# Optimization experiments

Measured on AMD Instinct MI355X. Metric: run time of the kernel, lower is better.

The kernel has to match this reference:

```python
import jax, jax.numpy as jnp
import numpy as np

BETA = 0.5
THR = 1.0
BN_EPS = 1e-5

@jax.custom_vjp
def spike(x):
    # heaviside fire: spk = 1[x > 0]
    return (x > 0).astype(x.dtype)

def _spike_fwd(x):
    return spike(x), x

def _spike_bwd(x, g):
    # snnTorch surrogate.atan(), alpha=2: grad = (alpha/2) / (1 + (pi/2*alpha*x)^2) = 1/(1+(pi*x)^2)
    return (g / (1.0 + (jnp.pi * x) ** 2),)

spike.defvjp(_spike_fwd, _spike_bwd)

def setup_inputs() -> dict:
    key = jax.random.key(0)
    ks = jax.random.split(key, 6)
    B, T, D, O = 512, 128, 512, 10
    data = jax.random.normal(ks[0], (B, T, D), dtype=jnp.float32)
    # deterministic Dropout(0.5) mask in {0, 2} (scaled by 1/keep_prob), time-major
    u = jax.random.uniform(ks[1], (T, B, D), dtype=jnp.float32)
    drop_mask = (u > 0.5).astype(jnp.float32) * 2.0
    W1 = jax.random.normal(ks[2], (D, D), dtype=jnp.float32) / np.sqrt(D)
    b1 = jax.random.normal(ks[3], (D,), dtype=jnp.float32) * 0.01
    gamma = jnp.ones((D,), dtype=jnp.float32)
    bn_beta = jnp.zeros((D,), dtype=jnp.float32)
    W2 = jax.random.normal(ks[4], (O, D), dtype=jnp.float32) / np.sqrt(D)
    b2 = jax.random.normal(ks[5], (O,), dtype=jnp.float32) * 0.01
    return {"data": data, "drop_mask": drop_mask, "W1": W1, "b1": b1,
            "gamma": gamma, "bn_beta": bn_beta, "W2": W2, "b2": b2}

def reference(data, drop_mask, W1, b1, gamma, bn_beta, W2, b2):
    B, T, D = data.shape
    O = W2.shape[0]
    xs = jnp.transpose(data, (1, 0, 2))  # [T, B, D] time-major

    def batchnorm(x):  # training-mode BatchNorm1d over batch dim
        mean = jnp.mean(x, axis=0)
        var = jnp.mean((x - mean) ** 2, axis=0)
        return gamma * (x - mean) * jax.lax.rsqrt(var + BN_EPS) + bn_beta

    def step(carry, inp):
        mem1, spk1, mem2, spk2 = carry
        xt, mt = inp
        cur1 = batchnorm((mt * xt) @ W1.T + b1)          # dropout -> linear -> BN
        mem1 = BETA * mem1 + cur1 - spk1 * THR           # Leaky, subtract reset
        spk1 = spike(mem1 - THR)
        cur2 = spk1 @ W2.T + b2
        mem2 = BETA * mem2 + cur2 - spk2 * THR
        spk2 = spike(mem2 - THR)
        return (mem1, spk1, mem2, spk2), spk2

    init = (jnp.zeros((B, D), data.dtype), jnp.zeros((B, D), data.dtype),
            jnp.zeros((B, O), data.dtype), jnp.zeros((B, O), data.dtype))
    _, spk_rec = jax.lax.scan(step, init, (xs, drop_mask))
    return spk_rec  # [T, B, out_size] == torch.stack(spk_rec)
```

## Files before the change

### kernel.cpp

```cpp
#include <hip/hip_runtime.h>
#include <math.h>

#define B_ 512
#define T_ 128
#define D_ 512
#define O_ 10

typedef unsigned int uint32;
typedef unsigned long long uint64;
typedef short bf16x8 __attribute__((ext_vector_type(8)));
typedef float f32x4 __attribute__((ext_vector_type(4)));

__device__ __forceinline__ uint32 bf16rne(float f) {
    uint32 u = __float_as_uint(f);
    return (u + 0x7FFFu + ((u >> 16) & 1u)) >> 16;
}
__device__ __forceinline__ float bf16f(uint32 h) { return __uint_as_float(h << 16); }

__device__ __forceinline__ uint32 pkbf16(float lo, float hi) {
    return bf16rne(lo) | (bf16rne(hi) << 16);
}

__device__ __forceinline__ void gload16_lds(const void* g, void* l) {
    __builtin_amdgcn_global_load_lds(
        (const __attribute__((address_space(1))) unsigned int*)g,
        (__attribute__((address_space(3))) unsigned int*)l, 16, 0, 0);
}

__global__ __launch_bounds__(256)
void presplitW_kernel(const float* __restrict__ W1, unsigned short* __restrict__ Wsp)
{
    const int idx = blockIdx.x * 256 + threadIdx.x;
    const float4 v = *(const float4*)(W1 + (size_t)idx * 4);
    float vv[4] = {v.x, v.y, v.z, v.w};
    uint32 c0[4], c1[4], c2[4];
#pragma unroll
    for (int i = 0; i < 4; ++i) {
        c0[i] = bf16rne(vv[i]);
        float r = vv[i] - bf16f(c0[i]);
        c1[i] = bf16rne(r);
        float r2 = r - bf16f(c1[i]);
        c2[i] = bf16rne(r2);
    }
    const size_t base = (size_t)idx * 4;
    uint2 w;
    w.x = c0[0] | (c0[1] << 16); w.y = c0[2] | (c0[3] << 16);
    *(uint2*)(Wsp + base) = w;
    w.x = c1[0] | (c1[1] << 16); w.y = c1[2] | (c1[3] << 16);
    *(uint2*)(Wsp + 262144 + base) = w;
    w.x = c2[0] | (c2[1] << 16); w.y = c2[2] | (c2[3] << 16);
    *(uint2*)(Wsp + 524288 + base) = w;
}

#define SPW 32
#define SPL (128*SPW)

__global__ __launch_bounds__(256)
void gemm1_kernel(const float* __restrict__ data, const float* __restrict__ drop,
                  const unsigned short* __restrict__ Wsp, const float* __restrict__ b1,
                  float* __restrict__ hbuf, double* __restrict__ pSum,
                  double* __restrict__ pSq, int t0, int Tc)
{
    __shared__ __align__(16) unsigned short As3[3 * SPL];
    __shared__ __align__(16) unsigned short Ws3[3 * SPL];

    const int tid = threadIdx.x;
    const int bid = blockIdx.x;
    const int xcd = bid & 7;
    const int rest = bid >> 3;
    const int yy = rest & 3;
    const int g = (rest >> 2) * 8 + xcd;

    const int R = g * 128;
    const int tc = R >> 9;
    const int b_base = R & 511;
    const int t = t0 + tc;
    const int d0 = yy * 128;

    const int w = tid >> 6;
    const int lane = tid & 63;
    const int wm = w & 1, wn = w >> 1;
    const int q = lane >> 4, r16 = lane & 15;

    f32x4 acc[4][4];
#pragma unroll
    for (int i = 0; i < 4; ++i)
#pragma unroll
        for (int j = 0; j < 4; ++j) acc[i][j] = (f32x4){0.f, 0.f, 0.f, 0.f};

    int dstA[2];
    const float* dsrc[2];
    const float* msrc[2];
#pragma unroll
    for (int i = 0; i < 2; ++i) {
        const int p = tid + i * 256;
        const int m = p >> 2;
        const int qg = p & 3;
        dstA[i] = m * SPW + (qg ^ ((m >> 1) & 3)) * 8;
        dsrc[i] = data + ((size_t)(b_base + m) * T_ + t) * D_ + qg * 8;
        msrc[i] = drop + ((size_t)t * B_ + b_base + m) * D_ + qg * 8;
    }
    float4 dR[2][2], mR[2][2];
#pragma unroll
    for (int i = 0; i < 2; ++i) {
        dR[i][0] = *(const float4*)(dsrc[i]);
        dR[i][1] = *(const float4*)(dsrc[i] + 4);
        mR[i][0] = *(const float4*)(msrc[i]);
        mR[i][1] = *(const float4*)(msrc[i] + 4);
    }

    for (int k0 = 0; k0 < 512; k0 += 32) {
#pragma unroll
        for (int i = 0; i < 6; ++i) {
            const int p = tid + i * 256;
            const int s = p >> 9;
            const int rem = p & 511;
            const int n = rem >> 2;
            const int qs = rem & 3;
            const int qg = qs ^ ((n >> 1) & 3);
            gload16_lds(Wsp + (size_t)s * 262144 + (size_t)(d0 + n) * 512 + k0 + qg * 8,
                        &Ws3[(size_t)p * 8]);
        }
#pragma unroll
        for (int i = 0; i < 2; ++i) {
            float vv[8] = {dR[i][0].x*mR[i][0].x, dR[i][0].y*mR[i][0].y,
                           dR[i][0].z*mR[i][0].z, dR[i][0].w*mR[i][0].w,
                           dR[i][1].x*mR[i][1].x, dR[i][1].y*mR[i][1].y,
                           dR[i][1].z*mR[i][1].z, dR[i][1].w*mR[i][1].w};
            uint32 q0[4], q1[4], q2[4];
#pragma unroll
            for (int pr = 0; pr < 4; ++pr) {
                const float a = vv[2*pr], b = vv[2*pr+1];
                q0[pr] = pkbf16(a, b);
                const float ra = a - __uint_as_float(q0[pr] << 16);
                const float rb = b - __uint_as_float(q0[pr] & 0xFFFF0000u);
                q1[pr] = pkbf16(ra, rb);
                const float sa = ra - __uint_as_float(q1[pr] << 16);
                const float sb = rb - __uint_as_float(q1[pr] & 0xFFFF0000u);
                q2[pr] = pkbf16(sa, sb);
            }
            uint4 pk;
            pk.x = q0[0]; pk.y = q0[1]; pk.z = q0[2]; pk.w = q0[3];
            *(uint4*)(&As3[dstA[i]]) = pk;
            pk.x = q1[0]; pk.y = q1[1]; pk.z = q1[2]; pk.w = q1[3];
            *(uint4*)(&As3[SPL + dstA[i]]) = pk;
            pk.x = q2[0]; pk.y = q2[1]; pk.z = q2[2]; pk.w = q2[3];
            *(uint4*)(&As3[2*SPL + dstA[i]]) = pk;
        }
        __syncthreads();

        const int qa = q ^ ((r16 >> 1) & 3);
        bf16x8 af[4][3], bfr[4][3];
#pragma unroll
        for (int mt = 0; mt < 4; ++mt)
#pragma unroll
            for (int s = 0; s < 3; ++s)
                af[mt][s] = *(const bf16x8*)(&As3[s*SPL + (wm*64 + mt*16 + r16)*SPW + qa*8]);
#pragma unroll
        for (int nt = 0; nt < 4; ++nt)
#pragma unroll
            for (int s = 0; s < 3; ++s)
                bfr[nt][s] = *(const bf16x8*)(&Ws3[s*SPL + (wn*64 + nt*16 + r16)*SPW + qa*8]);

        if (k0 + 32 < 512) {
            const int kn = k0 + 32;
#pragma unroll
            for (int i = 0; i < 2; ++i) {
                dR[i][0] = *(const float4*)(dsrc[i] + kn);
                dR[i][1] = *(const float4*)(dsrc[i] + kn + 4);
                mR[i][0] = *(const float4*)(msrc[i] + kn);
                mR[i][1] = *(const float4*)(msrc[i] + kn + 4);
            }
        }

#define PRODUCT(SA, SB)                                                          \
        {                                                                        \
            _Pragma("unroll")                                                    \
            for (int mt = 0; mt < 4; ++mt) {                                     \
                _Pragma("unroll")                                                \
                for (int nt = 0; nt < 4; ++nt)                                   \
                    acc[mt][nt] = __builtin_amdgcn_mfma_f32_16x16x32_bf16(       \
                        af[mt][SA], bfr[nt][SB], acc[mt][nt], 0, 0, 0);          \
            }                                                                    \
        }
        PRODUCT(0, 0)
        PRODUCT(0, 1)
        PRODUCT(1, 0)
        PRODUCT(1, 1)
        PRODUCT(0, 2)
        PRODUCT(2, 0)
#undef PRODUCT
        __syncthreads();
    }

    float b1c[4];
#pragma unroll
    for (int nt = 0; nt < 4; ++nt) b1c[nt] = b1[d0 + wn*64 + nt*16 + r16];

    double sd[4], sq[4];
#pragma unroll
    for (int nt = 0; nt < 4; ++nt) { sd[nt] = 0.0; sq[nt] = 0.0; }

#pragma unroll
    for (int mt = 0; mt < 4; ++mt)
#pragma unroll
        for (int r = 0; r < 4; ++r) {
            const int row = R + wm*64 + mt*16 + q*4 + r;
            float* op = hbuf + (size_t)row * D_ + d0 + wn*64 + r16;
#pragma unroll
            for (int nt = 0; nt < 4; ++nt) {
                const float hf = acc[mt][nt][r] + b1c[nt];
                op[nt*16] = hf;
                const double dh = (double)hf;
                sd[nt] += dh;
                sq[nt] = fma(dh, dh, sq[nt]);
            }
        }
#pragma unroll
    for (int nt = 0; nt < 4; ++nt) {
        sd[nt] += __shfl_xor(sd[nt], 16); sd[nt] += __shfl_xor(sd[nt], 32);
        sq[nt] += __shfl_xor(sq[nt], 16); sq[nt] += __shfl_xor(sq[nt], 32);
    }
    double* dsh = (double*)&As3[0];
    __syncthreads();
    if (q == 0) {
#pragma unroll
        for (int nt = 0; nt < 4; ++nt) {
            dsh[(w*64 + nt*16 + r16)*2 + 0] = sd[nt];
            dsh[(w*64 + nt*16 + r16)*2 + 1] = sq[nt];
        }
    }
    __syncthreads();
    if (tid < 128) {
        const int col = tid;
        const int gg = col >> 6, c = col & 63;
        const double S = dsh[((2*gg)*64 + c)*2 + 0] + dsh[((2*gg+1)*64 + c)*2 + 0];
        const double Q = dsh[((2*gg)*64 + c)*2 + 1] + dsh[((2*gg+1)*64 + c)*2 + 1];
        const int bt = b_base >> 7;
        pSum[((size_t)(bt*Tc + tc))*D_ + d0 + col] = S;
        pSq [((size_t)(bt*Tc + tc))*D_ + d0 + col] = Q;
    }
}

__global__ __launch_bounds__(256)
void finalize_kernel(const double* __restrict__ pSum, const double* __restrict__ pSq,
                     const float* __restrict__ gamma, const float* __restrict__ bn_beta,
                     float* __restrict__ scaleArr, float* __restrict__ shiftArr, int Tc)
{
    const int tc = blockIdx.x;
    const int d = blockIdx.y * 256 + threadIdx.x;
    double S = 0.0, Q = 0.0;
#pragma unroll
    for (int bt = 0; bt < 4; ++bt) {
        S += pSum[((size_t)(bt * Tc + tc)) * D_ + d];
        Q += pSq [((size_t)(bt * Tc + tc)) * D_ + d];
    }
    const double mean = S / (double)B_;
    const double var  = Q / (double)B_ - mean * mean;
    const double rs   = 1.0 / sqrt(var + 1e-5);
    const double gm   = (double)gamma[d] * rs;
    scaleArr[tc * D_ + d] = (float)gm;
    shiftArr[tc * D_ + d] = (float)((double)bn_beta[d] - gm * mean);
}

__global__ __launch_bounds__(256)
void scanA_kernel(const float* __restrict__ hbuf, const float* __restrict__ scaleArr,
                  const float* __restrict__ shiftArr, uint64* __restrict__ spkM,
                  float* __restrict__ sMem1, float* __restrict__ sSpk1, int t0, int Tc)
{
    const int e = blockIdx.x * 256 + threadIdx.x;
    const int d = e & 511;
    const int lane = threadIdx.x & 63;
    const int mword = (e >> 6);

    float m1, s1;
    if (t0 == 0) { m1 = 0.f; s1 = 0.f; }
    else { m1 = sMem1[e]; s1 = sSpk1[e]; }

    float hv[4], sc[4], sf[4];
#pragma unroll
    for (int j = 0; j < 4; ++j) {
        const int tcj = (j < Tc) ? j : (Tc - 1);
        hv[j] = hbuf[(size_t)tcj * (B_ * D_) + e];
        sc[j] = scaleArr[tcj * D_ + d];
        sf[j] = shiftArr[tcj * D_ + d];
    }

    for (int tc = 0; tc < Tc; tc += 4) {
        float hvN[4], scN[4], sfN[4];
#pragma unroll
        for (int j = 0; j < 4; ++j) {
            int tn = tc + 4 + j; tn = (tn < Tc) ? tn : (Tc - 1);
            hvN[j] = hbuf[(size_t)tn * (B_ * D_) + e];
            scN[j] = scaleArr[tn * D_ + d];
            sfN[j] = shiftArr[tn * D_ + d];
        }
#pragma unroll
        for (int j = 0; j < 4; ++j) {
            if (tc + j < Tc) {
                const float cur1 = fmaf(sc[j], hv[j], sf[j]);
                m1 = fmaf(0.5f, m1, cur1) - s1;
                s1 = ((m1 - 1.0f) > 0.f) ? 1.f : 0.f;
                const uint64 mask = __ballot(s1 == 1.f);
                if (lane == 0)
                    spkM[(size_t)(tc + j) * (B_ * 8) + mword] = mask;
            }
        }
#pragma unroll
        for (int j = 0; j < 4; ++j) { hv[j] = hvN[j]; sc[j] = scN[j]; sf[j] = sfN[j]; }
    }

    sMem1[e] = m1;
    sSpk1[e] = s1;
}

__global__ __launch_bounds__(256)
void gemm2_kernel(const uint64* __restrict__ spkM, const float* __restrict__ W2,
                  const float* __restrict__ b2, float* __restrict__ cur2)
{
    const int g = blockIdx.x * 256 + threadIdx.x;
    const int row = g >> 3;
    const int i = g & 7;
    const unsigned char* sp = (const unsigned char*)spkM;

    float P[8][O_];
#pragma unroll
    for (int c = 0; c < 8; ++c) {
        const uint32 byte = sp[(size_t)row * 64 + c * 8 + i];
        float f[8];
#pragma unroll
        for (int j = 0; j < 8; ++j)
            f[j] = (byte & (1u << j)) ? 1.0f : 0.0f;
#pragma unroll
        for (int o = 0; o < O_; ++o) {
            const float* wp = W2 + o * D_ + (i + 8 * c) * 8;
            const float4 wa = *(const float4*)(wp);
            const float4 wb = *(const float4*)(wp + 4);
            float v = f[0] * wa.x;
            v = fmaf(f[1], wa.y, v); v = fmaf(f[2], wa.z, v); v = fmaf(f[3], wa.w, v);
            v = fmaf(f[4], wb.x, v); v = fmaf(f[5], wb.y, v); v = fmaf(f[6], wb.z, v);
            v = fmaf(f[7], wb.w, v);
            P[c][o] = v;
        }
    }

    float p[O_];
#pragma unroll
    for (int o = 0; o < O_; ++o) {
        const float a1 = P[0][o] + P[4][o];
        const float a2 = P[2][o] + P[6][o];
        const float a3 = P[1][o] + P[5][o];
        const float a4 = P[3][o] + P[7][o];
        p[o] = (a1 + a2) + (a3 + a4);
    }
#pragma unroll
    for (int o = 0; o < O_; ++o) {
        p[o] += __shfl_xor(p[o], 4);
        p[o] += __shfl_xor(p[o], 2);
        p[o] += __shfl_xor(p[o], 1);
    }

    float out0 = 0.f, out1 = 0.f;
#pragma unroll
    for (int o = 0; o < 8; ++o)
        if (i == o) out0 = p[o] + b2[o];
    if (i == 0) out1 = p[8] + b2[8];
    if (i == 1) out1 = p[9] + b2[9];
    cur2[(size_t)row * O_ + i] = out0;
    if (i < 2)
        cur2[(size_t)row * O_ + 8 + i] = out1;
}

__global__ __launch_bounds__(256)
void scanB_kernel(const float* __restrict__ cur2, float* __restrict__ out,
                  float* __restrict__ sMem2, float* __restrict__ sSpk2, int t0, int Tc)
{
    const int idx = blockIdx.x * 256 + threadIdx.x;
    float mem2, spk2;
    if (t0 == 0) { mem2 = 0.f; spk2 = 0.f; }
    else { mem2 = sMem2[idx]; spk2 = sSpk2[idx]; }

    float v[4], vn[4];
#pragma unroll
    for (int j = 0; j < 4; ++j) v[j] = cur2[(size_t)j * (B_ * O_) + idx];

    for (int tg = 0; tg < Tc; tg += 4) {
        if (tg + 4 < Tc) {
#pragma unroll
            for (int j = 0; j < 4; ++j)
                vn[j] = cur2[(size_t)(tg + 4 + j) * (B_ * O_) + idx];
        }
#pragma unroll
        for (int j = 0; j < 4; ++j) {
            mem2 = fmaf(0.5f, mem2, v[j]) - spk2;
            spk2 = ((mem2 - 1.0f) > 0.f) ? 1.f : 0.f;
            out[(size_t)(t0 + tg + j) * (B_ * O_) + idx] = spk2;
        }
#pragma unroll
        for (int j = 0; j < 4; ++j) v[j] = vn[j];
    }
    sMem2[idx] = mem2;
    sSpk2[idx] = spk2;
}

extern "C" void kernel_launch(void* const* d_in, const int* in_sizes, int n_in,
                              void* d_out, int out_size, void* d_ws, size_t ws_size,
                              hipStream_t stream) {
    const float* data    = (const float*)d_in[0];
    const float* drop    = (const float*)d_in[1];
    const float* W1      = (const float*)d_in[2];
    const float* b1      = (const float*)d_in[3];
    const float* gamma   = (const float*)d_in[4];
    const float* bn_beta = (const float*)d_in[5];
    const float* W2      = (const float*)d_in[6];
    const float* b2      = (const float*)d_in[7];
    float* out = (float*)d_out;

    const size_t fixedBytes = 1572864 + 2*1048576 + 2*20480;
    const size_t perT = 1048576 + 32768 + 20480 + 4096 + 32768;
    int Tc = T_;
    while (Tc > 2 && fixedBytes + (size_t)Tc * perT > ws_size) Tc >>= 1;

    char* p = (char*)d_ws;
    double* pSum    = (double*)p; p += (size_t)4 * Tc * D_ * 8;
    double* pSq     = (double*)p; p += (size_t)4 * Tc * D_ * 8;
    float* hbuf     = (float*)p; p += (size_t)Tc * B_ * D_ * 4;
    float* scaleArr = (float*)p; p += (size_t)Tc * D_ * 4;
    float* shiftArr = (float*)p; p += (size_t)Tc * D_ * 4;
    float* sMem1    = (float*)p; p += (size_t)B_ * D_ * 4;
    float* sSpk1    = (float*)p; p += (size_t)B_ * D_ * 4;
    float* sMem2    = (float*)p; p += (size_t)B_ * O_ * 4;
    float* sSpk2    = (float*)p; p += (size_t)B_ * O_ * 4;
    float* cur2     = (float*)p; p += (size_t)Tc * B_ * O_ * 4;
    unsigned short* Wsp = (unsigned short*)p; p += (size_t)3 * D_ * D_ * 2;
    uint64* spkM    = (uint64*)p; p += (size_t)Tc * B_ * 8 * 8;

    presplitW_kernel<<<256, 256, 0, stream>>>(W1, Wsp);

    for (int t0 = 0; t0 < T_; t0 += Tc) {
        gemm1_kernel<<<Tc * 16, 256, 0, stream>>>(data, drop, Wsp, b1, hbuf,
                                                  pSum, pSq, t0, Tc);
        finalize_kernel<<<dim3(Tc, D_ / 256), 256, 0, stream>>>(
            pSum, pSq, gamma, bn_beta, scaleArr, shiftArr, Tc);
        scanA_kernel<<<(B_ * D_) / 256, 256, 0, stream>>>(hbuf, scaleArr, shiftArr, spkM,
                                                          sMem1, sSpk1, t0, Tc);
        gemm2_kernel<<<Tc * 16, 256, 0, stream>>>(spkM, W2, b2, cur2);
        scanB_kernel<<<20, 256, 0, stream>>>(cur2, out, sMem2, sSpk2, t0, Tc);
    }
}
```

Baseline: 510.3 us.

## Double-buffer W1 LDS tiles in gemm1 and raise MFMA wave priority

The W1 split-bf16 tiles are now double-buffered in shared memory. The next k-slice's global-to-LDS loads are issued before the current slice is computed, so fetch latency overlaps the MFMA work. The two __syncthreads per step become a raw s_waitcnt lgkmcnt(0) plus s_barrier pair, and s_setprio is raised around the MFMA block. This doubles W LDS usage, which may lower occupancy. Nothing explicitly waits on vmcnt for the LDS-DMA loads before the buffer is read, so correctness depends on compiler-inserted waits.

```diff
diff --git a/kernel.cpp b/kernel.cpp
--- a/kernel.cpp
+++ b/kernel.cpp
@@ -62,7 +62,7 @@
                   double* __restrict__ pSq, int t0, int Tc)
 {
     __shared__ __align__(16) unsigned short As3[3 * SPL];
-    __shared__ __align__(16) unsigned short Ws3[3 * SPL];
+    __shared__ __align__(16) unsigned short Ws3[2][3 * SPL];
 
     const int tid = threadIdx.x;
     const int bid = blockIdx.x;
@@ -100,6 +100,24 @@
         dsrc[i] = data + ((size_t)(b_base + m) * T_ + t) * D_ + qg * 8;
         msrc[i] = drop + ((size_t)t * B_ + b_base + m) * D_ + qg * 8;
     }
+
+#define STAGE_W(K0, BUF)                                                        \
+    {                                                                           \
+        _Pragma("unroll")                                                       \
+        for (int i_ = 0; i_ < 6; ++i_) {                                        \
+            const int p_ = tid + i_ * 256;                                      \
+            const int s_ = p_ >> 9;                                             \
+            const int rem_ = p_ & 511;                                          \
+            const int n_ = rem_ >> 2;                                           \
+            const int qs_ = rem_ & 3;                                           \
+            const int qg_ = qs_ ^ ((n_ >> 1) & 3);                              \
+            gload16_lds(Wsp + (size_t)s_ * 262144 + (size_t)(d0 + n_) * 512     \
+                            + (K0) + qg_ * 8,                                   \
+                        &Ws3[BUF][(size_t)p_ * 8]);                             \
+        }                                                                       \
+    }
+
+    STAGE_W(0, 0);
     float4 dR[2][2], mR[2][2];
 #pragma unroll
     for (int i = 0; i < 2; ++i) {
@@ -109,18 +127,11 @@
         mR[i][1] = *(const float4*)(msrc[i] + 4);
     }
 
-    for (int k0 = 0; k0 < 512; k0 += 32) {
-#pragma unroll
-        for (int i = 0; i < 6; ++i) {
-            const int p = tid + i * 256;
-            const int s = p >> 9;
-            const int rem = p & 511;
-            const int n = rem >> 2;
-            const int qs = rem & 3;
-            const int qg = qs ^ ((n >> 1) & 3);
-            gload16_lds(Wsp + (size_t)s * 262144 + (size_t)(d0 + n) * 512 + k0 + qg * 8,
-                        &Ws3[(size_t)p * 8]);
-        }
+    int cur = 0;
+    for (int ks = 0; ks < 16; ++ks) {
+        const int k0 = ks * 32;
+        if (ks < 15) STAGE_W(k0 + 32, cur ^ 1);
+
 #pragma unroll
         for (int i = 0; i < 2; ++i) {
             float vv[8] = {dR[i][0].x*mR[i][0].x, dR[i][0].y*mR[i][0].y,
@@ -147,22 +158,8 @@
             pk.x = q2[0]; pk.y = q2[1]; pk.z = q2[2]; pk.w = q2[3];
             *(uint4*)(&As3[2*SPL + dstA[i]]) = pk;
         }
-        __syncthreads();
-
-        const int qa = q ^ ((r16 >> 1) & 3);
-        bf16x8 af[4][3], bfr[4][3];
-#pragma unroll
-        for (int mt = 0; mt < 4; ++mt)
-#pragma unroll
-            for (int s = 0; s < 3; ++s)
-                af[mt][s] = *(const bf16x8*)(&As3[s*SPL + (wm*64 + mt*16 + r16)*SPW + qa*8]);
-#pragma unroll
-        for (int nt = 0; nt < 4; ++nt)
-#pragma unroll
-            for (int s = 0; s < 3; ++s)
-                bfr[nt][s] = *(const bf16x8*)(&Ws3[s*SPL + (wn*64 + nt*16 + r16)*SPW + qa*8]);
-
-        if (k0 + 32 < 512) {
+
+        if (ks < 15) {
             const int kn = k0 + 32;
 #pragma unroll
             for (int i = 0; i < 2; ++i) {
@@ -173,6 +170,23 @@
             }
         }
 
+        asm volatile("s_waitcnt lgkmcnt(0)" ::: "memory");
+        asm volatile("s_barrier" ::: "memory");
+
+        const int qa = q ^ ((r16 >> 1) & 3);
+        bf16x8 af[4][3], bfr[4][3];
+#pragma unroll
+        for (int mt = 0; mt < 4; ++mt)
+#pragma unroll
+            for (int s = 0; s < 3; ++s)
+                af[mt][s] = *(const bf16x8*)(&As3[s*SPL + (wm*64 + mt*16 + r16)*SPW + qa*8]);
+#pragma unroll
+        for (int nt = 0; nt < 4; ++nt)
+#pragma unroll
+            for (int s = 0; s < 3; ++s)
+                bfr[nt][s] = *(const bf16x8*)(&Ws3[cur][s*SPL + (wn*64 + nt*16 + r16)*SPW + qa*8]);
+
+        __builtin_amdgcn_s_setprio(1);
 #define PRODUCT(SA, SB)                                                          \
         {                                                                        \
             _Pragma("unroll")                                                    \
@@ -190,8 +204,12 @@
         PRODUCT(0, 2)
         PRODUCT(2, 0)
 #undef PRODUCT
-        __syncthreads();
-    }
+        __builtin_amdgcn_s_setprio(0);
+
+        asm volatile("s_barrier" ::: "memory");
+        cur ^= 1;
+    }
+#undef STAGE_W
 
     float b1c[4];
 #pragma unroll
```

After: 519.7 us. About the same (+1.8%).
